# Performance work log

Hardware: AMD Instinct MI355X
Metric: run time of the kernel (lower is better)

Reference implementation:

```python
import jax, jax.numpy as jnp
import numpy as np

N, E, K, C, NB, G = 10000, 320000, 10, 32, 8, 8
RMAX, AVG = 5.0, 32.0
L_OF_M = np.array([0,1,1,1,2,2,2,2,2,3,3,3,3,3,3,3])
BLOCKS = [(0,1),(1,4),(4,9),(9,16)]


def _sph(u):
    # real spherical harmonics l=0..3, e3nn 'component' normalization (sum_m Y_lm^2 = 2l+1)
    x, y, z = u[:,0], u[:,1], u[:,2]
    s3=3**0.5; s5=5**0.5; s15=15**0.5; s105=105**0.5
    s35_8=(35.0/8.0)**0.5; s21_8=(21.0/8.0)**0.5; s7=7**0.5
    return jnp.stack([
        jnp.ones_like(x),
        s3*x, s3*y, s3*z,
        s15*x*y, s15*y*z, 0.5*s5*(3*z*z-1.0), s15*x*z, 0.5*s15*(x*x-y*y),
        s35_8*y*(3*x*x-y*y), s105*x*y*z, s21_8*y*(5*z*z-1.0),
        0.5*s7*z*(5*z*z-3.0), s21_8*x*(5*z*z-1.0), 0.5*s105*z*(x*x-y*y),
        s35_8*x*(x*x-3*y*y)], axis=-1)


def _radial(r):
    # Bessel basis * polynomial cutoff (p=5)
    n = jnp.arange(1, NB+1, dtype=r.dtype)
    bess = jnp.sqrt(2.0/RMAX)*jnp.sin(n*jnp.pi*r[:,None]/RMAX)/r[:,None]
    t = r/RMAX; p = 5.0
    env = 1.0 - (p+1)*(p+2)/2*t**5 + p*(p+2)*t**6 - p*(p+1)/2*t**7
    env = jnp.where(r < RMAX, env, 0.0)
    return bess*env[:,None]


def _interact(scal, ea, ef, snd, rcv, mws, Wl, n_nodes):
    h = ef
    for W in mws[:-1]:
        h = jax.nn.silu(h @ W)
    tw = (h @ mws[-1]).reshape(-1, C, 4)[:, :, L_OF_M]          # [E,C,16] per-(channel,l) tp weights
    mji = scal[snd][:, :, None] * tw * ea[:, None, :]            # per-edge CG-style tensor product
    msg = jax.ops.segment_sum(mji, rcv, num_segments=n_nodes) / AVG
    return jnp.concatenate([jnp.einsum('ncm,cd->ndm', msg[:, :, a:b], Wl[l])
                            for l, (a, b) in enumerate(BLOCKS)], axis=-1)


def _forward(positions, node_attrs, shifts, edge_index, batch, num_graphs,
             atomic_energies, W_emb, Wup1, M1a, M1b, M1c, M1d, Wl1, Wprod1,
             Wup2, M2a, M2b, M2c, M2d, Wl2, Wprod2, Wsc2, wr1, Wr2a, wr2b):
    snd, rcv = edge_index[0], edge_index[1]
    vec = positions[rcv] - positions[snd] + shifts
    r = jnp.sqrt(jnp.sum(vec*vec, -1) + 1e-12)
    ea = _sph(vec / r[:, None])           # [E,16]
    ef = _radial(r)                       # [E,8]
    nf0 = node_attrs @ W_emb              # node embedding [N,C]
    A1 = _interact(nf0 @ Wup1, ea, ef, snd, rcv, (M1a, M1b, M1c, M1d), Wl1, positions.shape[0])
    c1 = jnp.einsum('nk,kct->nct', node_attrs, Wprod1)          # element-dep product-basis coeffs
    a0 = A1[:, :, 0]
    nf1 = A1 * (c1[..., 0] + c1[..., 1]*a0 + c1[..., 2]*a0*a0)[:, :, None]  # correlation-3 product
    A2 = _interact(nf1[:, :, 0] @ Wup2, ea, ef, snd, rcv, (M2a, M2b, M2c, M2d), Wl2, positions.shape[0])
    pl = jnp.stack([jnp.sum(A2[:, :, a:b]**2, -1) for a, b in BLOCKS], -1)  # [N,C,4] invariants
    c2 = jnp.einsum('nk,kct->nct', node_attrs, Wprod2)
    nf2 = jnp.sum(c2*pl, -1) + jnp.einsum('nk,nc,kcd->nd', node_attrs, nf1[:, :, 0], Wsc2)
    e0 = node_attrs @ atomic_energies
    e1 = nf1[:, :, 0] @ wr1
    e2 = jax.nn.silu(nf2 @ Wr2a) @ wr2b
    node_energy = e0 + e1 + e2
    total = jax.ops.segment_sum(node_energy, batch, num_segments=num_graphs)
    return total, node_energy


def setup_inputs():
    key = jax.random.key(0)
    ks = jax.random.split(key, 24)
    s = 0.1
    inp = {}
    inp['positions'] = jax.random.normal(ks[0], (N, 3), jnp.float32)
    inp['node_attrs'] = jax.nn.one_hot(jax.random.randint(ks[1], (N,), 0, K), K, dtype=jnp.float32)
    inp['shifts'] = jnp.zeros((E, 3), jnp.float32)
    inp['edge_index'] = jax.random.randint(ks[2], (2, E), 0, N)
    inp['batch'] = jnp.sort(jax.random.randint(ks[3], (N,), 0, G))
    inp['num_graphs'] = G
    inp['atomic_energies'] = jax.random.normal(ks[4], (K,), jnp.float32)
    inp['W_emb'] = s*jax.random.normal(ks[5], (K, C), jnp.float32)
    inp['Wup1'] = s*jax.random.normal(ks[6], (C, C), jnp.float32)
    inp['M1a'] = s*jax.random.normal(ks[7], (NB, 64), jnp.float32)
    inp['M1b'] = s*jax.random.normal(ks[8], (64, 64), jnp.float32)
    inp['M1c'] = s*jax.random.normal(ks[9], (64, 64), jnp.float32)
    inp['M1d'] = s*jax.random.normal(ks[10], (64, C*4), jnp.float32)
    inp['Wl1'] = s*jax.random.normal(ks[11], (4, C, C), jnp.float32)
    inp['Wprod1'] = s*jax.random.normal(ks[12], (K, C, 3), jnp.float32)
    inp['Wup2'] = s*jax.random.normal(ks[13], (C, C), jnp.float32)
    inp['M2a'] = s*jax.random.normal(ks[14], (NB, 64), jnp.float32)
    inp['M2b'] = s*jax.random.normal(ks[15], (64, 64), jnp.float32)
    inp['M2c'] = s*jax.random.normal(ks[16], (64, 64), jnp.float32)
    inp['M2d'] = s*jax.random.normal(ks[17], (64, C*4), jnp.float32)
    inp['Wl2'] = s*jax.random.normal(ks[18], (4, C, C), jnp.float32)
    inp['Wprod2'] = s*jax.random.normal(ks[19], (K, C, 4), jnp.float32)
    inp['Wsc2'] = s*jax.random.normal(ks[20], (K, C, C), jnp.float32)
    inp['wr1'] = s*jax.random.normal(ks[21], (C,), jnp.float32)
    inp['Wr2a'] = s*jax.random.normal(ks[22], (C, 16), jnp.float32)
    inp['wr2b'] = s*jax.random.normal(ks[23], (16,), jnp.float32)
    return inp


def reference(positions, node_attrs, shifts, edge_index, batch, num_graphs,
              atomic_energies, W_emb, Wup1, M1a, M1b, M1c, M1d, Wl1, Wprod1,
              Wup2, M2a, M2b, M2c, M2d, Wl2, Wprod2, Wsc2, wr1, Wr2a, wr2b):
    def efn(pos):
        tot, ne = _forward(pos, node_attrs, shifts, edge_index, batch, num_graphs,
                           atomic_energies, W_emb, Wup1, M1a, M1b, M1c, M1d, Wl1, Wprod1,
                           Wup2, M2a, M2b, M2c, M2d, Wl2, Wprod2, Wsc2, wr1, Wr2a, wr2b)
        return jnp.sum(tot), (tot, ne)
    (_, (total, node_energy)), g = jax.value_and_grad(efn, has_aux=True)(positions)
    forces = -g  # forces = -dE/dpositions as in get_outputs
    return total, node_energy, forces
```

## Files before the change

### kernel.cpp

```cpp
#include <hip/hip_runtime.h>
#include <math.h>

#define NN 10000
#define NE 320000
#define KS 10
#define CC 32
#define GG 8
#define NTAB 2048
#define TROW 320
#define RMAXf 5.0f
#define AVGf 32.0f

#define OF_TAB 0
#define SZ_TAB ((NTAB + 1) * TROW)
#define OF_GEO (OF_TAB + SZ_TAB)
#define OF_SND (OF_GEO + 4 * NE)
#define OF_SPK (OF_SND + NE)
#define OF_RCSR (OF_SPK + NE)
#define OF_YE (OF_RCSR + NE)
#define OF_SC1 (OF_YE + 16 * NE)
#define OF_SP (OF_SC1 + KS * CC)
#define OF_RE (OF_SP + NN)
#define OF_UE (OF_RE + NE)
#define OF_GV (OF_UE + 3 * NE)
#define OF_A0 (OF_GV + 3 * NE)
#define OF_NF1 (OF_A0 + NN * CC)
#define OF_SCAL2 (OF_NF1 + NN * CC)
#define OF_NEP (OF_SCAL2 + NN * CC)
#define OF_GM2T (OF_NEP + NN)
#define OF_GNF1P (OF_GM2T + NN * CC * 16)
#define OF_GS1 (OF_GNF1P + NN * CC)
#define OF_ROWS (OF_GS1 + NN * CC)
#define OF_DEG (OF_ROWS + NN + 1)
#define OF_CUR (OF_DEG + NN)
#define OF_GSC2 (OF_CUR + NN)
#define OF_END (OF_GSC2 + NN * CC)

__device__ __forceinline__ int lm_of(int m) { return (m == 0) ? 0 : (m < 4) ? 1 : (m < 9) ? 2 : 3; }

__device__ __forceinline__ void sph16(float x, float y, float z, float* Y) {
    const float s3 = 1.7320508075688772f, s5 = 2.23606797749979f, s15 = 3.872983346207417f,
                s105 = 10.246950765959598f, s358 = 2.091650066335189f,
                s218 = 1.6201851746019651f, s7 = 2.6457513110645907f;
    Y[0] = 1.f;
    Y[1] = s3 * x; Y[2] = s3 * y; Y[3] = s3 * z;
    Y[4] = s15 * x * y; Y[5] = s15 * y * z; Y[6] = 0.5f * s5 * (3.f * z * z - 1.f);
    Y[7] = s15 * x * z; Y[8] = 0.5f * s15 * (x * x - y * y);
    Y[9] = s358 * y * (3.f * x * x - y * y);
    Y[10] = s105 * x * y * z;
    Y[11] = s218 * y * (5.f * z * z - 1.f);
    Y[12] = 0.5f * s7 * z * (5.f * z * z - 3.f);
    Y[13] = s218 * x * (5.f * z * z - 1.f);
    Y[14] = 0.5f * s105 * z * (x * x - y * y);
    Y[15] = s358 * x * (x * x - 3.f * y * y);
}

__device__ __forceinline__ void sph16_grad(float x, float y, float z, float* Dx, float* Dy, float* Dz) {
    const float s3 = 1.7320508075688772f, s5 = 2.23606797749979f, s15 = 3.872983346207417f,
                s105 = 10.246950765959598f, s358 = 2.091650066335189f,
                s218 = 1.6201851746019651f, s7 = 2.6457513110645907f;
    Dx[0] = 0; Dy[0] = 0; Dz[0] = 0;
    Dx[1] = s3; Dy[1] = 0; Dz[1] = 0;
    Dx[2] = 0; Dy[2] = s3; Dz[2] = 0;
    Dx[3] = 0; Dy[3] = 0; Dz[3] = s3;
    Dx[4] = s15 * y; Dy[4] = s15 * x; Dz[4] = 0;
    Dx[5] = 0; Dy[5] = s15 * z; Dz[5] = s15 * y;
    Dx[6] = 0; Dy[6] = 0; Dz[6] = 3.f * s5 * z;
    Dx[7] = s15 * z; Dy[7] = 0; Dz[7] = s15 * x;
    Dx[8] = s15 * x; Dy[8] = -s15 * y; Dz[8] = 0;
    Dx[9] = 6.f * s358 * x * y; Dy[9] = 3.f * s358 * (x * x - y * y); Dz[9] = 0;
    Dx[10] = s105 * y * z; Dy[10] = s105 * x * z; Dz[10] = s105 * x * y;
    Dx[11] = 0; Dy[11] = s218 * (5.f * z * z - 1.f); Dz[11] = 10.f * s218 * y * z;
    Dx[12] = 0; Dy[12] = 0; Dz[12] = 0.5f * s7 * (15.f * z * z - 3.f);
    Dx[13] = s218 * (5.f * z * z - 1.f); Dy[13] = 0; Dz[13] = 10.f * s218 * x * z;
    Dx[14] = s105 * x * z; Dy[14] = -s105 * y * z; Dz[14] = 0.5f * s105 * (x * x - y * y);
    Dx[15] = 3.f * s358 * (x * x - y * y); Dy[15] = -6.f * s358 * x * y; Dz[15] = 0;
}

__global__ void k_species(const float* __restrict__ na, int* __restrict__ sp) {
    int n = blockIdx.x * blockDim.x + threadIdx.x;
    if (n >= NN) return;
    int k = 0;
    for (int j = 0; j < KS; j++)
        if (na[n * KS + j] > 0.5f) k = j;
    sp[n] = k;
}

__global__ void k_scal1(const float* __restrict__ Wemb, const float* __restrict__ Wup1, float* __restrict__ st) {
    int i = threadIdx.x;
    if (i >= KS * CC) return;
    int k = i / CC, c = i % CC;
    float s = 0;
    for (int j = 0; j < CC; j++) s += Wemb[k * CC + j] * Wup1[j * CC + c];
    st[i] = s;
}

__global__ void k_table(const float* __restrict__ M1a, const float* __restrict__ M1b,
                        const float* __restrict__ M1c, const float* __restrict__ M1d,
                        const float* __restrict__ M2a, const float* __restrict__ M2b,
                        const float* __restrict__ M2c, const float* __restrict__ M2d,
                        float* __restrict__ tab) {
    const double PI = 3.14159265358979323846;
    int row = blockIdx.x;
    int j = threadIdx.x;
    __shared__ float sR[8], sdR[8];
    __shared__ float sA[64], sdA[64], sB[64], sdB[64];
    if (j < 8) {
        double r = (double)row * ((double)RMAXf / NTAB);
        if (r < 1e-6) r = 1e-6;
        double a = (double)(j + 1) * PI / (double)RMAXf;
        double env = 0.0, denv = 0.0;
        if (row < NTAB) {
            double t = r / (double)RMAXf;
            double t4 = t * t * t * t;
            env = 1.0 - 21.0 * t4 * t + 35.0 * t4 * t * t - 15.0 * t4 * t * t * t;
            denv = (-105.0 * t4 + 210.0 * t4 * t - 105.0 * t4 * t * t) / (double)RMAXf;
        }
        double pref = sqrt(2.0 / (double)RMAXf);
        double s = sin(a * r), cg = cos(a * r);
        double bess = pref * s / r;
        double dbess = pref * (a * cg / r - s / (r * r));
        sR[j] = (float)(bess * env);
        sdR[j] = (float)(dbess * env + bess * denv);
    }
    __syncthreads();
    size_t rb = (size_t)row * TROW;

    {
        float p = 0, dp = 0;
        for (int i = 0; i < 8; i++) { float w = M1a[i * 64 + j]; p += sR[i] * w; dp += sdR[i] * w; }
        float sg = 1.f / (1.f + expf(-p));
        sB[j] = p * sg; sdB[j] = dp * sg * (1.f + p * (1.f - sg));
    }
    __syncthreads();
    {
        float p = 0, dp = 0;
        for (int i = 0; i < 64; i++) { float w = M1b[i * 64 + j]; p += sB[i] * w; dp += sdB[i] * w; }
        float sg = 1.f / (1.f + expf(-p));
        sA[j] = p * sg; sdA[j] = dp * sg * (1.f + p * (1.f - sg));
    }
    __syncthreads();
    {
        float p = 0, dp = 0;
        for (int i = 0; i < 64; i++) { float w = M1c[i * 64 + j]; p += sA[i] * w; dp += sdA[i] * w; }
        float sg = 1.f / (1.f + expf(-p));
        sB[j] = p * sg; sdB[j] = dp * sg * (1.f + p * (1.f - sg));
    }
    __syncthreads();
    #pragma unroll
    for (int t2 = 0; t2 < 2; t2++) {
        int o = j + t2 * 64;
        if ((o & 3) == 0) {
            float p = 0, dp = 0;
            for (int i = 0; i < 64; i++) { float w = M1d[i * 128 + o]; p += sB[i] * w; dp += sdB[i] * w; }
            int c = o >> 2;
            tab[rb + c] = p;
            tab[rb + 32 + c] = dp;
        }
    }
    __syncthreads();

    {
        float p = 0, dp = 0;
        for (int i = 0; i < 8; i++) { float w = M2a[i * 64 + j]; p += sR[i] * w; dp += sdR[i] * w; }
        float sg = 1.f / (1.f + expf(-p));
        sB[j] = p * sg; sdB[j] = dp * sg * (1.f + p * (1.f - sg));
    }
    __syncthreads();
    {
        float p = 0, dp = 0;
        for (int i = 0; i < 64; i++) { float w = M2b[i * 64 + j]; p += sB[i] * w; dp += sdB[i] * w; }
        float sg = 1.f / (1.f + expf(-p));
        sA[j] = p * sg; sdA[j] = dp * sg * (1.f + p * (1.f - sg));
    }
    __syncthreads();
    {
        float p = 0, dp = 0;
        for (int i = 0; i < 64; i++) { float w = M2c[i * 64 + j]; p += sA[i] * w; dp += sdA[i] * w; }
        float sg = 1.f / (1.f + expf(-p));
        sB[j] = p * sg; sdB[j] = dp * sg * (1.f + p * (1.f - sg));
    }
    __syncthreads();
    #pragma unroll
    for (int t2 = 0; t2 < 2; t2++) {
        int o = j + t2 * 64;
        float p = 0, dp = 0;
        for (int i = 0; i < 64; i++) { float w = M2d[i * 128 + o]; p += sB[i] * w; dp += sdB[i] * w; }
        tab[rb + 64 + o] = p;
        tab[rb + 192 + o] = dp;
    }
}

__global__ void k_geom(const float* __restrict__ pos, const float* __restrict__ shifts,
                       const int* __restrict__ ei, float* __restrict__ re,
                       float* __restrict__ ue, int* __restrict__ deg) {
    int e = blockIdx.x * 256 + threadIdx.x;
    if (e >= NE) return;
    int s = ei[e], t = ei[NE + e];
    float vx = pos[3 * t] - pos[3 * s] + shifts[3 * e];
    float vy = pos[3 * t + 1] - pos[3 * s + 1] + shifts[3 * e + 1];
    float vz = pos[3 * t + 2] - pos[3 * s + 2] + shifts[3 * e + 2];
    float r = sqrtf(vx * vx + vy * vy + vz * vz + 1e-12f);
    float inv = 1.f / r;
    re[e] = r;
    ue[3 * e] = vx * inv;
    ue[3 * e + 1] = vy * inv;
    ue[3 * e + 2] = vz * inv;
    atomicAdd(&deg[t], 1);
}

__global__ void k_scan(const int* __restrict__ deg, int* __restrict__ rows, int* __restrict__ cur) {
    __shared__ int part[1024];
    int t = threadIdx.x;
    const int per = (NN + 1023) / 1024;
    int base = t * per;
    int s = 0;
    for (int i = 0; i < per; i++) {
        int idx = base + i;
        if (idx < NN) s += deg[idx];
    }
    part[t] = s;
    __syncthreads();
    for (int off = 1; off < 1024; off <<= 1) {
        int v = (t >= off) ? part[t - off] : 0;
        __syncthreads();
        part[t] += v;
        __syncthreads();
    }
    int run = (t == 0) ? 0 : part[t - 1];
    for (int i = 0; i < per; i++) {
        int idx = base + i;
        if (idx < NN) {
            rows[idx] = run;
            cur[idx] = run;
            run += deg[idx];
        }
    }
    if (t == 1023) rows[NN] = run;
}

__global__ void k_fill(const int* __restrict__ ei, const int* __restrict__ sp,
                       const float* __restrict__ re, const float* __restrict__ ue,
                       int* __restrict__ cur, int* __restrict__ snd, int* __restrict__ spk,
                       float* __restrict__ rcsr, float4* __restrict__ geo,
                       float* __restrict__ YE) {
    int e = blockIdx.x * 256 + threadIdx.x;
    if (e >= NE) return;
    int s = ei[e], t = ei[NE + e];
    int p = atomicAdd(&cur[t], 1);
    float ux = ue[3 * e], uy = ue[3 * e + 1], uz = ue[3 * e + 2];
    snd[p] = s;
    spk[p] = sp[s];
    rcsr[p] = re[e];
    geo[p] = make_float4(re[e], ux, uy, uz);
    float Y[16];
    sph16(ux, uy, uz, Y);
    float4* yp = (float4*)&YE[(size_t)p * 16];
    yp[0] = make_float4(Y[0], Y[1], Y[2], Y[3]);
    yp[1] = make_float4(Y[4], Y[5], Y[6], Y[7]);
    yp[2] = make_float4(Y[8], Y[9], Y[10], Y[11]);
    yp[3] = make_float4(Y[12], Y[13], Y[14], Y[15]);
}

__global__ __launch_bounds__(256, 4)
void k_gather1(const int* __restrict__ rows, const int* __restrict__ spk,
               const float* __restrict__ rcsr, const int* __restrict__ sp,
               const float* __restrict__ sc1, const float* __restrict__ tab,
               const float* __restrict__ Wl1, const float* __restrict__ Wprod1,
               const float* __restrict__ Wup2, const float* __restrict__ wr1,
               const float* __restrict__ aE,
               float* __restrict__ a0s, float* __restrict__ nf1,
               float* __restrict__ scal2, float* __restrict__ nep) {
    __shared__ float red[4][CC];
    int wid = blockIdx.x;
    int tid = threadIdx.x;
    int wv = tid >> 6, lane = tid & 63, c = lane & 31, h = lane >> 5, hb = h << 5;
    int stream = wv * 2 + h;
    int r0 = rows[wid], dg = rows[wid + 1] - r0;
    float acc = 0.f;
    for (int j = stream; j < dg; j += 8) {
        int p = r0 + j;
        float r = rcsr[p];
        float scv = sc1[spk[p] * CC + c];
        float w1 = 0.f;
        if (r < RMAXf) {
            float tt = r * (NTAB / RMAXf);
            int i = (int)tt; if (i > NTAB - 1) i = NTAB - 1;
            float f = tt - (float)i;
            size_t b = (size_t)i * TROW + c;
            w1 = tab[b] * (1.f - f) + tab[b + TROW] * f;
        }
        acc += scv * w1;
    }
    acc += __shfl_xor(acc, 32, 64);
    if (h == 0) red[wv][c] = acc;
    __syncthreads();
    if (wv != 0) return;
    acc = red[0][c] + red[1][c] + red[2][c] + red[3][c];
    float a0 = 0.f;
    for (int d = 0; d < CC; d++) a0 += __shfl(acc, hb + d, 64) * Wl1[d * CC + c];
    a0 *= (1.f / AVGf);
    int k = sp[wid];
    const float* cp = &Wprod1[(k * CC + c) * 3];
    float nf = a0 * (cp[0] + cp[1] * a0 + cp[2] * a0 * a0);
    float s2 = 0.f;
    for (int d = 0; d < CC; d++) s2 += __shfl(nf, hb + d, 64) * Wup2[d * CC + c];
    float t1 = nf * wr1[c];
    for (int m = 16; m >= 1; m >>= 1) t1 += __shfl_xor(t1, m, 64);
    if (h == 0) {
        a0s[wid * CC + c] = a0;
        nf1[wid * CC + c] = nf;
        scal2[wid * CC + c] = s2;
        if (c == 0) nep[wid] = aE[k] + t1;
    }
}

__global__ __launch_bounds__(256, 4)
void k_node2(const int* __restrict__ rows, const int* __restrict__ snd,
             const float* __restrict__ rcsr, const float* __restrict__ YE,
             const int* __restrict__ sp,
             const float* __restrict__ scal2, const float* __restrict__ tab,
             const float* __restrict__ Wl2, const float* __restrict__ Wprod2,
             const float* __restrict__ Wsc2, const float* __restrict__ nf1,
             const float* __restrict__ Wr2a, const float* __restrict__ wr2b,
             const float* __restrict__ wr1, const float* __restrict__ nep,
             const int* __restrict__ batch,
             float* __restrict__ gm2T, float* __restrict__ gnf1p,
             float* __restrict__ out_total, float* __restrict__ out_ne) {
    __shared__ float lds[4][16 * 32];
    int wid = blockIdx.x;
    int tid = threadIdx.x;
    int wv = tid >> 6, lane = tid & 63, c = lane & 31, h = lane >> 5, hb = h << 5;
    int stream = wv * 2 + h;
    int r0 = rows[wid], dg = rows[wid + 1] - r0;

    float S2r[16];
    #pragma unroll
    for (int m = 0; m < 16; m++) S2r[m] = 0.f;
    for (int j = stream; j < dg; j += 8) {
        int p = r0 + j;
        float r = rcsr[p];
        float sc = scal2[snd[p] * CC + c];
        float scw[4] = {0, 0, 0, 0};
        if (r < RMAXf) {
            float tt = r * (NTAB / RMAXf);
            int i = (int)tt; if (i > NTAB - 1) i = NTAB - 1;
            float f = tt - (float)i;
            size_t b = (size_t)i * TROW + 64 + c * 4;
            float4 t0 = *(const float4*)&tab[b];
            float4 t1 = *(const float4*)&tab[b + TROW];
            scw[0] = sc * (t0.x + (t1.x - t0.x) * f);
            scw[1] = sc * (t0.y + (t1.y - t0.y) * f);
            scw[2] = sc * (t0.z + (t1.z - t0.z) * f);
            scw[3] = sc * (t0.w + (t1.w - t0.w) * f);
        }
        const float4* yp = (const float4*)&YE[(size_t)p * 16];
        float4 y0 = yp[0], y1 = yp[1], y2 = yp[2], y3 = yp[3];
        float Y[16] = {y0.x, y0.y, y0.z, y0.w, y1.x, y1.y, y1.z, y1.w,
                       y2.x, y2.y, y2.z, y2.w, y3.x, y3.y, y3.z, y3.w};
        #pragma unroll
        for (int m = 0; m < 16; m++) S2r[m] += scw[lm_of(m)] * Y[m];
    }
    #pragma unroll
    for (int m = 0; m < 16; m++) S2r[m] += __shfl_xor(S2r[m], 32, 64);
    if (h == 0) {
        #pragma unroll
        for (int m = 0; m < 16; m++) lds[wv][m * 32 + c] = S2r[m];
    }
    __syncthreads();
    for (int idx = tid; idx < 512; idx += 256)
        lds[0][idx] += lds[1][idx] + lds[2][idx] + lds[3][idx];
    __syncthreads();
    if (wv != 0) return;

    int d = c;
    float A2r[16];
    #pragma unroll
    for (int m = 0; m < 16; m++) {
        const float* wl = &Wl2[lm_of(m) * CC * CC];
        float acc = 0;
        for (int cc = 0; cc < CC; cc++) acc += lds[0][m * 32 + cc] * wl[cc * CC + d];
        A2r[m] = acc * (1.f / AVGf);
    }
    float pl[4] = {0, 0, 0, 0};
    #pragma unroll
    for (int m = 0; m < 16; m++) pl[lm_of(m)] += A2r[m] * A2r[m];
    int k = sp[wid];
    const float* c2 = &Wprod2[(k * CC + d) * 4];
    float nf2 = c2[0] * pl[0] + c2[1] * pl[1] + c2[2] * pl[2] + c2[3] * pl[3];
    for (int cc = 0; cc < CC; cc++) nf2 += nf1[wid * CC + cc] * Wsc2[((size_t)k * CC + cc) * CC + d];
    int jj = d & 15;
    float zj = 0;
    for (int dd = 0; dd < CC; dd++) zj += __shfl(nf2, hb + dd, 64) * Wr2a[dd * 16 + jj];
    float sg = 1.f / (1.f + expf(-zj));
    float e2p = (d < 16) ? zj * sg * wr2b[jj] : 0.f;
    float red = e2p;
    for (int m = 16; m >= 1; m >>= 1) red += __shfl_xor(red, m, 64);
    if (h == 0 && d == 0) {
        float ne = nep[wid] + red;
        out_ne[wid] = ne;
        atomicAdd(&out_total[batch[wid]], ne);
    }
    float gz = sg * (1.f + zj * (1.f - sg)) * wr2b[jj];
    float gn = 0;
    for (int j2 = 0; j2 < 16; j2++) gn += Wr2a[d * 16 + j2] * __shfl(gz, hb + j2, 64);
    if (h == 0) {
        #pragma unroll
        for (int m = 0; m < 16; m++) lds[0][m * 32 + d] = 2.f * A2r[m] * gn * c2[lm_of(m)];
    }
    float gmv[16];
    #pragma unroll
    for (int m = 0; m < 16; m++) {
        const float* wl = &Wl2[lm_of(m) * CC * CC + c * CC];
        float acc = 0;
        for (int dd = 0; dd < CC; dd++) acc += lds[0][m * 32 + dd] * wl[dd];
        gmv[m] = acc * (1.f / AVGf);
    }
    float g1 = wr1[c];
    for (int dd = 0; dd < CC; dd++) g1 += __shfl(gn, hb + dd, 64) * Wsc2[((size_t)k * CC + c) * CC + dd];
    if (h == 0) {
        #pragma unroll
        for (int m = 0; m < 16; m++) gm2T[(size_t)wid * 512 + c * 16 + m] = gmv[m];
        gnf1p[wid * CC + c] = g1;
    }
}

__global__ __launch_bounds__(256, 4)
void k_gbwd2(const int* __restrict__ rows, const int* __restrict__ snd,
             const float4* __restrict__ geo, const float* __restrict__ YE,
             const float* __restrict__ scal2, const float* __restrict__ tab,
             const float* __restrict__ gm2T,
             float* __restrict__ gsc2, float* __restrict__ gvcsr) {
    int wid = blockIdx.x;
    int tid = threadIdx.x;
    int wv = tid >> 6, lane = tid & 63, c = lane & 31, h = lane >> 5;
    int stream = wv * 2 + h;
    float gm[16];
    #pragma unroll
    for (int m = 0; m < 16; m++) gm[m] = gm2T[(size_t)wid * 512 + c * 16 + m];
    int r0 = rows[wid], dg = rows[wid + 1] - r0;
    for (int j = stream; j < dg; j += 8) {
        int p = r0 + j;
        float4 g4 = geo[p];
        int s = snd[p];
        float sc = scal2[s * CC + c];
        float r = g4.x, ux = g4.y, uy = g4.z, uz = g4.w;
        float w2[4] = {0, 0, 0, 0}, scw[4] = {0, 0, 0, 0}, sdw[4] = {0, 0, 0, 0};
        if (r < RMAXf) {
            float tt = r * (NTAB / RMAXf);
            int i = (int)tt; if (i > NTAB - 1) i = NTAB - 1;
            float f = tt - (float)i;
            size_t b = (size_t)i * TROW + 64 + c * 4;
            size_t b2 = (size_t)i * TROW + 192 + c * 4;
            float4 t0 = *(const float4*)&tab[b];
            float4 t1 = *(const float4*)&tab[b + TROW];
            float4 d0 = *(const float4*)&tab[b2];
            float4 d1 = *(const float4*)&tab[b2 + TROW];
            w2[0] = t0.x + (t1.x - t0.x) * f; w2[1] = t0.y + (t1.y - t0.y) * f;
            w2[2] = t0.z + (t1.z - t0.z) * f; w2[3] = t0.w + (t1.w - t0.w) * f;
            sdw[0] = sc * (d0.x + (d1.x - d0.x) * f); sdw[1] = sc * (d0.y + (d1.y - d0.y) * f);
            sdw[2] = sc * (d0.z + (d1.z - d0.z) * f); sdw[3] = sc * (d0.w + (d1.w - d0.w) * f);
            scw[0] = sc * w2[0]; scw[1] = sc * w2[1]; scw[2] = sc * w2[2]; scw[3] = sc * w2[3];
        }
        const float4* yp = (const float4*)&YE[(size_t)p * 16];
        float4 y0 = yp[0], y1 = yp[1], y2 = yp[2], y3 = yp[3];
        float Y[16] = {y0.x, y0.y, y0.z, y0.w, y1.x, y1.y, y1.z, y1.w,
                       y2.x, y2.y, y2.z, y2.w, y3.x, y3.y, y3.z, y3.w};
        float Dx[16], Dy[16], Dz[16];
        sph16_grad(ux, uy, uz, Dx, Dy, Dz);
        float gsc = 0, gdr = 0, gx = 0, gy = 0, gz = 0;
        #pragma unroll
        for (int m = 0; m < 16; m++) {
            float g = gm[m];
            int l = lm_of(m);
            float t = g * Y[m];
            gsc += t * w2[l];
            gdr += t * sdw[l];
            float gY = g * scw[l];
            gx += gY * Dx[m]; gy += gY * Dy[m]; gz += gY * Dz[m];
        }
        atomicAdd(&gsc2[s * CC + c], gsc);
        for (int m2 = 16; m2 >= 1; m2 >>= 1) {
            gdr += __shfl_xor(gdr, m2, 64);
            gx += __shfl_xor(gx, m2, 64);
            gy += __shfl_xor(gy, m2, 64);
            gz += __shfl_xor(gz, m2, 64);
        }
        if (c == 0) {
            float inv = 1.f / r;
            float dot = ux * gx + uy * gy + uz * gz;
            gvcsr[3 * p] = ux * gdr + (gx - ux * dot) * inv;
            gvcsr[3 * p + 1] = uy * gdr + (gy - uy * dot) * inv;
            gvcsr[3 * p + 2] = uz * gdr + (gz - uz * dot) * inv;
        }
    }
}

__global__ void k_node_bwd2(const float* __restrict__ gnf1p, const float* __restrict__ gsc2,
                            const float* __restrict__ Wup2, const float* __restrict__ a0s,
                            const int* __restrict__ sp, const float* __restrict__ Wprod1,
                            const float* __restrict__ Wl1, float* __restrict__ gS1) {
    int gid = blockIdx.x * 256 + threadIdx.x;
    int n = gid >> 5, c = gid & 31;
    if (n >= NN) return;
    int hb = threadIdx.x & 32;
    float g1 = gnf1p[n * CC + c];
    for (int dd = 0; dd < CC; dd++) g1 += gsc2[n * CC + dd] * Wup2[c * CC + dd];
    float a0 = a0s[n * CC + c];
    int k = sp[n];
    const float* cp = &Wprod1[(k * CC + c) * 3];
    float ga0 = g1 * (cp[0] + 2.f * cp[1] * a0 + 3.f * cp[2] * a0 * a0);
    float acc = 0;
    for (int dd = 0; dd < CC; dd++) acc += __shfl(ga0, hb + dd, 64) * Wl1[c * CC + dd];
    gS1[n * CC + c] = acc * (1.f / AVGf);
}

__global__ __launch_bounds__(256, 4)
void k_gbwd1(const int* __restrict__ rows, const int* __restrict__ snd,
             const int* __restrict__ spk, const float* __restrict__ rcsr,
             const float4* __restrict__ geo, const float* __restrict__ sc1,
             const float* __restrict__ tab, const float* __restrict__ gS1,
             const float* __restrict__ gvcsr, float* __restrict__ F) {
    int wid = blockIdx.x;
    int tid = threadIdx.x;
    int wv = tid >> 6, lane = tid & 63, c = lane & 31, h = lane >> 5;
    int stream = wv * 2 + h;
    int r0 = rows[wid], dg = rows[wid + 1] - r0;
    float gst = gS1[wid * CC + c];
    float ft = 0.f;
    for (int j = stream; j < dg; j += 8) {
        int p = r0 + j;
        float r = rcsr[p];
        int s = snd[p];
        float dw = 0.f;
        if (r < RMAXf) {
            float tt = r * (NTAB / RMAXf);
            int i = (int)tt; if (i > NTAB - 1) i = NTAB - 1;
            float f = tt - (float)i;
            size_t b = (size_t)i * TROW + 32 + c;
            dw = tab[b] * (1.f - f) + tab[b + TROW] * f;
        }
        float gdr = gst * sc1[spk[p] * CC + c] * dw;
        for (int m = 16; m >= 1; m >>= 1) gdr += __shfl_xor(gdr, m, 64);
        if (c < 3) {
            float4 g4 = geo[p];
            float u = (c == 0) ? g4.y : (c == 1) ? g4.z : g4.w;
            float gv = gvcsr[3 * p + c] + u * gdr;
            atomicAdd(&F[3 * s + c], gv);
            ft -= gv;
        }
    }
    if (c < 3) atomicAdd(&F[3 * wid + c], ft);
}

extern "C" void kernel_launch(void* const* d_in, const int* in_sizes, int n_in,
                              void* d_out, int out_size, void* d_ws, size_t ws_size,
                              hipStream_t stream) {
    const float* pos = (const float*)d_in[0];
    const float* na = (const float*)d_in[1];
    const float* shifts = (const float*)d_in[2];
    const int* ei = (const int*)d_in[3];
    const int* batch = (const int*)d_in[4];
    const float* aE = (const float*)d_in[6];
    const float* Wemb = (const float*)d_in[7];
    const float* Wup1 = (const float*)d_in[8];
    const float* M1a = (const float*)d_in[9];
    const float* M1b = (const float*)d_in[10];
    const float* M1c = (const float*)d_in[11];
    const float* M1d = (const float*)d_in[12];
    const float* Wl1 = (const float*)d_in[13];
    const float* Wprod1 = (const float*)d_in[14];
    const float* Wup2 = (const float*)d_in[15];
    const float* M2a = (const float*)d_in[16];
    const float* M2b = (const float*)d_in[17];
    const float* M2c = (const float*)d_in[18];
    const float* M2d = (const float*)d_in[19];
    const float* Wl2 = (const float*)d_in[20];
    const float* Wprod2 = (const float*)d_in[21];
    const float* Wsc2 = (const float*)d_in[22];
    const float* wr1 = (const float*)d_in[23];
    const float* Wr2a = (const float*)d_in[24];
    const float* wr2b = (const float*)d_in[25];

    float* ws = (float*)d_ws;
    float* tab = ws + OF_TAB;
    float4* geo = (float4*)(ws + OF_GEO);
    int* snd = (int*)(ws + OF_SND);
    int* spk = (int*)(ws + OF_SPK);
    float* rcsr = ws + OF_RCSR;
    float* YE = ws + OF_YE;
    float* sc1 = ws + OF_SC1;
    int* sp = (int*)(ws + OF_SP);
    float* re = ws + OF_RE;
    float* ue = ws + OF_UE;
    float* gv = ws + OF_GV;
    float* a0s = ws + OF_A0;
    float* nf1 = ws + OF_NF1;
    float* scal2 = ws + OF_SCAL2;
    float* nep = ws + OF_NEP;
    float* gm2T = ws + OF_GM2T;
    float* gnf1p = ws + OF_GNF1P;
    float* gS1 = ws + OF_GS1;
    int* rows = (int*)(ws + OF_ROWS);
    int* deg = (int*)(ws + OF_DEG);
    int* cur = (int*)(ws + OF_CUR);
    float* gsc2 = ws + OF_GSC2;

    float* out_total = (float*)d_out;
    float* out_ne = out_total + GG;
    float* out_F = out_ne + NN;

    hipMemsetAsync(d_out, 0, sizeof(float) * (GG + NN + 3 * NN), stream);
    hipMemsetAsync(deg, 0, sizeof(float) * (size_t)(OF_END - OF_DEG), stream);

    k_species<<<(NN + 255) / 256, 256, 0, stream>>>(na, sp);
    k_scal1<<<1, 320, 0, stream>>>(Wemb, Wup1, sc1);
    k_table<<<NTAB + 1, 64, 0, stream>>>(M1a, M1b, M1c, M1d, M2a, M2b, M2c, M2d, tab);
    k_geom<<<(NE + 255) / 256, 256, 0, stream>>>(pos, shifts, ei, re, ue, deg);
    k_scan<<<1, 1024, 0, stream>>>(deg, rows, cur);
    k_fill<<<(NE + 255) / 256, 256, 0, stream>>>(ei, sp, re, ue, cur, snd, spk, rcsr, geo, YE);
    k_gather1<<<NN, 256, 0, stream>>>(rows, spk, rcsr, sp, sc1, tab, Wl1, Wprod1,
                                      Wup2, wr1, aE, a0s, nf1, scal2, nep);
    k_node2<<<NN, 256, 0, stream>>>(rows, snd, rcsr, YE, sp, scal2, tab, Wl2,
                                    Wprod2, Wsc2, nf1, Wr2a, wr2b, wr1, nep, batch,
                                    gm2T, gnf1p, out_total, out_ne);
    k_gbwd2<<<NN, 256, 0, stream>>>(rows, snd, geo, YE, scal2, tab, gm2T, gsc2, gv);
    k_node_bwd2<<<NN / 8, 256, 0, stream>>>(gnf1p, gsc2, Wup2, a0s, sp, Wprod1, Wl1, gS1);
    k_gbwd1<<<NN, 256, 0, stream>>>(rows, snd, spk, rcsr, geo, sc1, tab, gS1, gv, out_F);
}
```

Measured before the change: 440.2 us.

## Fuse edge geometry into CSR fill, raise occupancy bounds, transpose gm2T layout

Edge geometry (distance and unit vector) is now computed directly in the CSR fill kernel, and the degree-count kernel only does the atomic increment. This removes the intermediate re/ue buffers and their write and re-read. Launch bounds on the three per-node gather kernels are raised from 4 to 8 blocks per SM, which may force the compiler into register spills. The gm2T gradient buffer is stored m-major so its per-channel writes and reads coalesce.

```diff
diff --git a/kernel.cpp b/kernel.cpp
--- a/kernel.cpp
+++ b/kernel.cpp
@@ -20,9 +20,7 @@
 #define OF_YE (OF_RCSR + NE)
 #define OF_SC1 (OF_YE + 16 * NE)
 #define OF_SP (OF_SC1 + KS * CC)
-#define OF_RE (OF_SP + NN)
-#define OF_UE (OF_RE + NE)
-#define OF_GV (OF_UE + 3 * NE)
+#define OF_GV (OF_SP + NN)
 #define OF_A0 (OF_GV + 3 * NE)
 #define OF_NF1 (OF_A0 + NN * CC)
 #define OF_SCAL2 (OF_NF1 + NN * CC)
@@ -191,22 +189,10 @@
     }
 }
 
-__global__ void k_geom(const float* __restrict__ pos, const float* __restrict__ shifts,
-                       const int* __restrict__ ei, float* __restrict__ re,
-                       float* __restrict__ ue, int* __restrict__ deg) {
+__global__ void k_deg(const int* __restrict__ ei, int* __restrict__ deg) {
     int e = blockIdx.x * 256 + threadIdx.x;
     if (e >= NE) return;
-    int s = ei[e], t = ei[NE + e];
-    float vx = pos[3 * t] - pos[3 * s] + shifts[3 * e];
-    float vy = pos[3 * t + 1] - pos[3 * s + 1] + shifts[3 * e + 1];
-    float vz = pos[3 * t + 2] - pos[3 * s + 2] + shifts[3 * e + 2];
-    float r = sqrtf(vx * vx + vy * vy + vz * vz + 1e-12f);
-    float inv = 1.f / r;
-    re[e] = r;
-    ue[3 * e] = vx * inv;
-    ue[3 * e + 1] = vy * inv;
-    ue[3 * e + 2] = vz * inv;
-    atomicAdd(&deg[t], 1);
+    atomicAdd(&deg[ei[NE + e]], 1);
 }
 
 __global__ void k_scan(const int* __restrict__ deg, int* __restrict__ rows, int* __restrict__ cur) {
@@ -239,20 +225,25 @@
     if (t == 1023) rows[NN] = run;
 }
 
-__global__ void k_fill(const int* __restrict__ ei, const int* __restrict__ sp,
-                       const float* __restrict__ re, const float* __restrict__ ue,
+__global__ void k_fill(const float* __restrict__ pos, const float* __restrict__ shifts,
+                       const int* __restrict__ ei, const int* __restrict__ sp,
                        int* __restrict__ cur, int* __restrict__ snd, int* __restrict__ spk,
                        float* __restrict__ rcsr, float4* __restrict__ geo,
                        float* __restrict__ YE) {
     int e = blockIdx.x * 256 + threadIdx.x;
     if (e >= NE) return;
     int s = ei[e], t = ei[NE + e];
+    float vx = pos[3 * t] - pos[3 * s] + shifts[3 * e];
+    float vy = pos[3 * t + 1] - pos[3 * s + 1] + shifts[3 * e + 1];
+    float vz = pos[3 * t + 2] - pos[3 * s + 2] + shifts[3 * e + 2];
+    float r = sqrtf(vx * vx + vy * vy + vz * vz + 1e-12f);
+    float inv = 1.f / r;
+    float ux = vx * inv, uy = vy * inv, uz = vz * inv;
     int p = atomicAdd(&cur[t], 1);
-    float ux = ue[3 * e], uy = ue[3 * e + 1], uz = ue[3 * e + 2];
     snd[p] = s;
     spk[p] = sp[s];
-    rcsr[p] = re[e];
-    geo[p] = make_float4(re[e], ux, uy, uz);
+    rcsr[p] = r;
+    geo[p] = make_float4(r, ux, uy, uz);
     float Y[16];
     sph16(ux, uy, uz, Y);
     float4* yp = (float4*)&YE[(size_t)p * 16];
@@ -262,7 +253,7 @@
     yp[3] = make_float4(Y[12], Y[13], Y[14], Y[15]);
 }
 
-__global__ __launch_bounds__(256, 4)
+__global__ __launch_bounds__(256, 8)
 void k_gather1(const int* __restrict__ rows, const int* __restrict__ spk,
                const float* __restrict__ rcsr, const int* __restrict__ sp,
                const float* __restrict__ sc1, const float* __restrict__ tab,
@@ -315,7 +306,7 @@
     }
 }
 
-__global__ __launch_bounds__(256, 4)
+__global__ __launch_bounds__(256, 8)
 void k_node2(const int* __restrict__ rows, const int* __restrict__ snd,
              const float* __restrict__ rcsr, const float* __restrict__ YE,
              const int* __restrict__ sp,
@@ -327,7 +318,7 @@
              const int* __restrict__ batch,
              float* __restrict__ gm2T, float* __restrict__ gnf1p,
              float* __restrict__ out_total, float* __restrict__ out_ne) {
-    __shared__ float lds[4][16 * 32];
+    __shared__ float lds[4][512];
     int wid = blockIdx.x;
     int tid = threadIdx.x;
     int wv = tid >> 6, lane = tid & 63, c = lane & 31, h = lane >> 5, hb = h << 5;
@@ -420,7 +411,7 @@
     for (int dd = 0; dd < CC; dd++) g1 += __shfl(gn, hb + dd, 64) * Wsc2[((size_t)k * CC + c) * CC + dd];
     if (h == 0) {
         #pragma unroll
-        for (int m = 0; m < 16; m++) gm2T[(size_t)wid * 512 + c * 16 + m] = gmv[m];
+        for (int m = 0; m < 16; m++) gm2T[(size_t)wid * 512 + m * 32 + c] = gmv[m];
         gnf1p[wid * CC + c] = g1;
     }
 }
@@ -437,7 +428,7 @@
     int stream = wv * 2 + h;
     float gm[16];
     #pragma unroll
-    for (int m = 0; m < 16; m++) gm[m] = gm2T[(size_t)wid * 512 + c * 16 + m];
+    for (int m = 0; m < 16; m++) gm[m] = gm2T[(size_t)wid * 512 + m * 32 + c];
     int r0 = rows[wid], dg = rows[wid + 1] - r0;
     for (int j = stream; j < dg; j += 8) {
         int p = r0 + j;
@@ -515,7 +506,7 @@
     gS1[n * CC + c] = acc * (1.f / AVGf);
 }
 
-__global__ __launch_bounds__(256, 4)
+__global__ __launch_bounds__(256, 8)
 void k_gbwd1(const int* __restrict__ rows, const int* __restrict__ snd,
              const int* __restrict__ spk, const float* __restrict__ rcsr,
              const float4* __restrict__ geo, const float* __restrict__ sc1,
@@ -591,8 +582,6 @@
     float* YE = ws + OF_YE;
     float* sc1 = ws + OF_SC1;
     int* sp = (int*)(ws + OF_SP);
-    float* re = ws + OF_RE;
-    float* ue = ws + OF_UE;
     float* gv = ws + OF_GV;
     float* a0s = ws + OF_A0;
     float* nf1 = ws + OF_NF1;
@@ -616,9 +605,9 @@
     k_species<<<(NN + 255) / 256, 256, 0, stream>>>(na, sp);
     k_scal1<<<1, 320, 0, stream>>>(Wemb, Wup1, sc1);
     k_table<<<NTAB + 1, 64, 0, stream>>>(M1a, M1b, M1c, M1d, M2a, M2b, M2c, M2d, tab);
-    k_geom<<<(NE + 255) / 256, 256, 0, stream>>>(pos, shifts, ei, re, ue, deg);
+    k_deg<<<(NE + 255) / 256, 256, 0, stream>>>(ei, deg);
     k_scan<<<1, 1024, 0, stream>>>(deg, rows, cur);
-    k_fill<<<(NE + 255) / 256, 256, 0, stream>>>(ei, sp, re, ue, cur, snd, spk, rcsr, geo, YE);
+    k_fill<<<(NE + 255) / 256, 256, 0, stream>>>(pos, shifts, ei, sp, cur, snd, spk, rcsr, geo, YE);
     k_gather1<<<NN, 256, 0, stream>>>(rows, spk, rcsr, sp, sc1, tab, Wl1, Wprod1,
                                       Wup2, wr1, aE, a0s, nf1, scal2, nep);
     k_node2<<<NN, 256, 0, stream>>>(rows, snd, rcsr, YE, sp, scal2, tab, Wl2,
```

Result: faster. 431.3 us (median of 2 runs) (-2.0%).
